# Performance work log

Measured on AMD Instinct MI355X. Metric: run time of the kernel, lower is better.

The kernel has to match this reference:

```python
import jax, jax.numpy as jnp
import numpy as np

D_MODEL, D_INNER, D_STATE, D_CONV, DT_RANK = 2048, 4096, 16, 4, 128
B, T = 2, 1024


def setup_inputs() -> dict:
    key = jax.random.key(0)
    ks = jax.random.split(key, 8)
    dt_init_std = DT_RANK ** -0.5
    # dt bias init per the torch code: inv softplus of dt in [dt_min, dt_max]
    dt = jnp.exp(jax.random.uniform(ks[6], (D_INNER,)) * (np.log(0.1) - np.log(0.001)) + np.log(0.001))
    dt = jnp.clip(dt, 1e-4, None)
    dt_proj_b = dt + jnp.log(-jnp.expm1(-dt))
    A_log = jnp.log(jnp.tile(jnp.arange(1, D_STATE + 1, dtype=jnp.float32)[None, :], (D_INNER, 1)))
    return {
        "x": jax.random.normal(ks[0], (B, T, D_MODEL), jnp.float32),
        "h": jnp.zeros((B, D_INNER, D_STATE), jnp.float32),
        "conv_cache": jnp.zeros((B, D_INNER, D_CONV - 1), jnp.float32),
        "in_proj_w": jax.random.normal(ks[1], (2 * D_INNER, D_MODEL), jnp.float32) * 0.02,
        "conv_w": jax.random.normal(ks[2], (D_INNER, D_CONV), jnp.float32) * (1.0 / np.sqrt(D_CONV)),
        "conv_b": jnp.zeros((D_INNER,), jnp.float32),
        "x_proj_w": jax.random.normal(ks[3], (DT_RANK + 2 * D_STATE, D_INNER), jnp.float32) * 0.02,
        "dt_proj_w": jax.random.uniform(ks[4], (D_INNER, DT_RANK), jnp.float32, -dt_init_std, dt_init_std),
        "dt_proj_b": dt_proj_b,
        "A_log": A_log,
        "D_param": jnp.ones((D_INNER,), jnp.float32),
        "out_proj_w": jax.random.normal(ks[5], (D_MODEL, D_INNER), jnp.float32) * 0.02,
    }


def _forward(x, h, conv_cache, in_proj_w, conv_w, conv_b, x_proj_w,
             dt_proj_w, dt_proj_b, A_log, D_param, out_proj_w):
    Tlen = x.shape[1]
    xz = x @ in_proj_w.T                                  # (B,T,2*d_inner)
    xi, z = jnp.split(xz, 2, axis=-1)
    # causal depthwise conv with cache: concat history then valid conv
    xc = jnp.concatenate([jnp.swapaxes(conv_cache, 1, 2), xi], axis=1)  # (B,T+3,d_inner)
    new_conv_cache = jnp.swapaxes(xc[:, -(D_CONV - 1):, :], 1, 2)       # (B,d_inner,3)
    xconv = sum(xc[:, k:k + Tlen, :] * conv_w[:, k] for k in range(D_CONV)) + conv_b
    xs = jax.nn.silu(xconv)                               # (B,T,d_inner)
    # SSM params per step
    dbc = xs @ x_proj_w.T                                 # (B,T,dt_rank+2n)
    delta, Bm, Cm = jnp.split(dbc, [DT_RANK, DT_RANK + D_STATE], axis=-1)
    delta = jax.nn.softplus(delta @ dt_proj_w.T + dt_proj_b)  # (B,T,d_inner)
    A = -jnp.exp(A_log)                                   # (d_inner,n)
    dA = jnp.exp(jnp.einsum('btd,dn->btdn', delta, A))    # (B,T,d,n)
    dBx = jnp.einsum('btd,btn,btd->btdn', delta, Bm, xs)  # (B,T,d,n)

    def step(hc, inp):
        dA_t, dBx_t, C_t = inp
        hc = dA_t * hc + dBx_t                            # (B,d,n)
        return hc, jnp.einsum('bdn,bn->bd', hc, C_t)

    h_last, ys = jax.lax.scan(
        step, h,
        (jnp.moveaxis(dA, 1, 0), jnp.moveaxis(dBx, 1, 0), jnp.moveaxis(Cm, 1, 0)))
    y = jnp.moveaxis(ys, 0, 1) + D_param * xs             # (B,T,d_inner)
    out = (y * jax.nn.silu(z)) @ out_proj_w.T             # (B,T,d_model)
    return out, h_last, new_conv_cache


def reference(x, h, conv_cache, in_proj_w, conv_w, conv_b, x_proj_w,
              dt_proj_w, dt_proj_b, A_log, D_param, out_proj_w):
    return _forward(x, h, conv_cache, in_proj_w, conv_w, conv_b, x_proj_w,
                    dt_proj_w, dt_proj_b, A_log, D_param, out_proj_w)
```

## Files before the change

### kernel.cpp

```cpp
#include <hip/hip_runtime.h>
#include <hip/hip_bf16.h>
#include <math.h>

#define D_MODEL 2048
#define D_INNER 4096
#define D_STATE 16
#define D_CONV  4
#define DT_RANK 128
#define NB      2
#define TT      1024
#define M_TOT   (NB * TT)
#define NC      16
#define CL      64
#define TC      16

typedef __bf16 bf16x8_t __attribute__((ext_vector_type(8)));
typedef float  f32x4_t  __attribute__((ext_vector_type(4)));

__global__ __launch_bounds__(256) void fused_cast(
    const float* __restrict__ x,  const float* __restrict__ wi,
    const float* __restrict__ wo, const float* __restrict__ wx,
    const float* __restrict__ wdt,
    __bf16* __restrict__ x16,  __bf16* __restrict__ wi16,
    __bf16* __restrict__ wo16, __bf16* __restrict__ wx16,
    __bf16* __restrict__ wdt16, __bf16* __restrict__ dbc16)
{
    const size_t g = (size_t)blockIdx.x * 256 + threadIdx.x;
    const float* src; __bf16* dst; size_t off;
    if      (g < 524288)  { src = x;   dst = x16;   off = g; }
    else if (g < 2621440) { src = wi;  dst = wi16;  off = g - 524288; }
    else if (g < 3670016) { src = wo;  dst = wo16;  off = g - 2621440; }
    else if (g < 3801088) { off = g - 3670016; dst = wx16;
                            src = (g < 3751936) ? wx : nullptr; }
    else if (g < 3866624) { src = wdt; dst = wdt16; off = g - 3801088; }
    else                  { src = nullptr; dst = dbc16; off = g - 3866624; }

    bf16x8_t v;
    if (src) {
        const float4 f0 = ((const float4*)src)[2 * off];
        const float4 f1 = ((const float4*)src)[2 * off + 1];
        v[0] = (__bf16)f0.x; v[1] = (__bf16)f0.y; v[2] = (__bf16)f0.z; v[3] = (__bf16)f0.w;
        v[4] = (__bf16)f1.x; v[5] = (__bf16)f1.y; v[6] = (__bf16)f1.z; v[7] = (__bf16)f1.w;
    } else {
        v = (bf16x8_t)(__bf16)0.f;
    }
    ((bf16x8_t*)dst)[off] = v;
}

__global__ __launch_bounds__(256) void cast_dt16(
    const float* __restrict__ dbc, __bf16* __restrict__ dt16)
{
    int i = blockIdx.x * 256 + threadIdx.x;
    int row = i >> 4, chunk = i & 15;
    const float* s = dbc + (size_t)row * 160 + chunk * 8;
    const float4 f0 = *(const float4*)s;
    const float4 f1 = *(const float4*)(s + 4);
    bf16x8_t v;
    v[0] = (__bf16)f0.x; v[1] = (__bf16)f0.y; v[2] = (__bf16)f0.z; v[3] = (__bf16)f0.w;
    v[4] = (__bf16)f1.x; v[5] = (__bf16)f1.y; v[6] = (__bf16)f1.z; v[7] = (__bf16)f1.w;
    ((bf16x8_t*)(dt16 + (size_t)row * 128))[chunk] = v;
}

template <int EPI, typename OutT>
__global__ __launch_bounds__(256) void gemm_bf16_nt(
    const __bf16* __restrict__ A, int lda,
    const __bf16* __restrict__ W, int ldw,
    OutT* __restrict__ C, int ldc,
    int Kloop, int Nmax, const float* __restrict__ bias)
{
    __shared__ __bf16 As[128 * 32];
    __shared__ __bf16 Bs[128 * 32];

    const int tid  = threadIdx.x;
    const int wave = tid >> 6;
    const int lane = tid & 63;
    const int m0 = blockIdx.y * 128;
    const int n0 = blockIdx.x * 128;
    const int mw = (wave >> 1) * 64;
    const int nw = (wave & 1) * 64;
    const int koff = blockIdx.z * Kloop;

    f32x4_t acc[4][4] = {};

    const int g0 = wave * 2;
    const int rA = g0 * 16 + (lane >> 2);
    const int kk = (lane & 3) * 8;

    const __bf16* gA0 = A + (size_t)(m0 + rA) * lda + kk + koff;
    const __bf16* gA1 = gA0 + (size_t)16 * lda;
    const __bf16* gB0 = W + (size_t)(n0 + rA) * ldw + kk + koff;
    const __bf16* gB1 = gB0 + (size_t)16 * ldw;

    __bf16* lA0 = &As[(size_t)g0 * 512];
    __bf16* lA1 = &As[(size_t)(g0 + 1) * 512];
    __bf16* lB0 = &Bs[(size_t)g0 * 512];
    __bf16* lB1 = &Bs[(size_t)(g0 + 1) * 512];

    const int fr = lane & 15;
    const int fk = (lane >> 4) * 8;

    for (int k0 = 0; k0 < Kloop; k0 += 32) {
        __builtin_amdgcn_global_load_lds(
            (const __attribute__((address_space(1))) void*)(gA0 + k0),
            (__attribute__((address_space(3))) void*)lA0, 16, 0, 0);
        __builtin_amdgcn_global_load_lds(
            (const __attribute__((address_space(1))) void*)(gA1 + k0),
            (__attribute__((address_space(3))) void*)lA1, 16, 0, 0);
        __builtin_amdgcn_global_load_lds(
            (const __attribute__((address_space(1))) void*)(gB0 + k0),
            (__attribute__((address_space(3))) void*)lB0, 16, 0, 0);
        __builtin_amdgcn_global_load_lds(
            (const __attribute__((address_space(1))) void*)(gB1 + k0),
            (__attribute__((address_space(3))) void*)lB1, 16, 0, 0);
        __syncthreads();

        bf16x8_t av[4], bv[4];
#pragma unroll
        for (int mt = 0; mt < 4; mt++)
            av[mt] = *(const bf16x8_t*)&As[(mw + mt * 16 + fr) * 32 + fk];
#pragma unroll
        for (int nt = 0; nt < 4; nt++)
            bv[nt] = *(const bf16x8_t*)&Bs[(nw + nt * 16 + fr) * 32 + fk];

#pragma unroll
        for (int mt = 0; mt < 4; mt++)
#pragma unroll
            for (int nt = 0; nt < 4; nt++)
                acc[mt][nt] = __builtin_amdgcn_mfma_f32_16x16x32_bf16(
                    av[mt], bv[nt], acc[mt][nt], 0, 0, 0);
        __syncthreads();
    }

    const int cn = n0 + nw + (lane & 15);
    const int rb = m0 + mw + (lane >> 4) * 4;
#pragma unroll
    for (int mt = 0; mt < 4; mt++)
#pragma unroll
        for (int nt = 0; nt < 4; nt++) {
            const int n = cn + nt * 16;
            if (n >= Nmax) continue;
#pragma unroll
            for (int r = 0; r < 4; r++) {
                float v = acc[mt][nt][r];
                OutT* p = &C[(size_t)(rb + mt * 16 + r) * ldc + n];
                if (EPI == 1) {
                    v += bias[n];
                    v = (v > 20.f) ? v : log1pf(__expf(v));
                    *p = (OutT)v;
                } else if (EPI == 2) {
                    atomicAdd((float*)p, v);
                } else {
                    *p = (OutT)v;
                }
            }
        }
}

__global__ __launch_bounds__(256) void conv_silu(
    const __bf16* __restrict__ xz16,
    const float* __restrict__ conv_cache,
    const float* __restrict__ conv_w,
    const float* __restrict__ conv_b,
    __bf16* __restrict__ xs16,
    float* __restrict__ cc_out)
{
    const int b  = blockIdx.z;
    const int d  = blockIdx.y * 256 + threadIdx.x;
    const int t0 = blockIdx.x * TC;

    const float4 w  = *(const float4*)&conv_w[d * 4];
    const float bias = conv_b[d];

    float v[TC + 3];
    if (t0 == 0) {
        v[0] = conv_cache[(b * D_INNER + d) * 3 + 0];
        v[1] = conv_cache[(b * D_INNER + d) * 3 + 1];
        v[2] = conv_cache[(b * D_INNER + d) * 3 + 2];
    } else {
        v[0] = (float)xz16[(size_t)(b * TT + t0 - 3) * 8192 + d];
        v[1] = (float)xz16[(size_t)(b * TT + t0 - 2) * 8192 + d];
        v[2] = (float)xz16[(size_t)(b * TT + t0 - 1) * 8192 + d];
    }
#pragma unroll
    for (int k = 0; k < TC; k++)
        v[k + 3] = (float)xz16[(size_t)(b * TT + t0 + k) * 8192 + d];

#pragma unroll
    for (int k = 0; k < TC; k++) {
        float c = v[k] * w.x + v[k + 1] * w.y + v[k + 2] * w.z + v[k + 3] * w.w + bias;
        float s = c / (1.f + __expf(-c));
        xs16[(size_t)(b * TT + t0 + k) * 4096 + d] = (__bf16)s;
    }

    if (t0 + TC == TT) {
        cc_out[(b * D_INNER + d) * 3 + 0] = v[TC];
        cc_out[(b * D_INNER + d) * 3 + 1] = v[TC + 1];
        cc_out[(b * D_INNER + d) * 3 + 2] = v[TC + 2];
    }
}

__global__ __launch_bounds__(256) void scan_phase_a(
    const float* __restrict__ delta_p,
    const float* __restrict__ dbc,
    const __bf16* __restrict__ xs16,
    const float* __restrict__ A_log,
    float* __restrict__ P,
    float* __restrict__ S)
{
    const int idx = blockIdx.x * 256 + threadIdx.x;
    const int sub = idx & 3;
    const int d   = (idx >> 2) & 4095;
    const int c   = (idx >> 14) & (NC - 1);
    const int b   = idx >> 18;

    const float4 Af = *(const float4*)&A_log[d * 16 + sub * 4];
    const float Ad0 = -__expf(Af.x), Ad1 = -__expf(Af.y);
    const float Ad2 = -__expf(Af.z), Ad3 = -__expf(Af.w);

    const int t0 = c * CL;
    const float*  pdelta = delta_p + (size_t)(b * TT + t0) * 4096 + d;
    const __bf16* px     = xs16 + (size_t)(b * TT + t0) * 4096 + d;
    const float*  pB     = dbc + ((size_t)b * TT + t0) * 160 + 128 + sub * 4;

    float h0 = 0.f, h1 = 0.f, h2 = 0.f, h3 = 0.f, sd = 0.f;
    for (int t = 0; t < CL; t++) {
        const float delta = pdelta[(size_t)t * 4096];
        const float xv    = (float)px[(size_t)t * 4096];
        const float4 Bv   = *(const float4*)&pB[(size_t)t * 160];
        const float dx = delta * xv;
        h0 = __expf(delta * Ad0) * h0 + dx * Bv.x;
        h1 = __expf(delta * Ad1) * h1 + dx * Bv.y;
        h2 = __expf(delta * Ad2) * h2 + dx * Bv.z;
        h3 = __expf(delta * Ad3) * h3 + dx * Bv.w;
        sd += delta;
    }
    const size_t o = ((size_t)(b * NC + c) * 4096 + d) * 16 + sub * 4;
    *(float4*)&P[o] = make_float4(__expf(Ad0 * sd), __expf(Ad1 * sd),
                                  __expf(Ad2 * sd), __expf(Ad3 * sd));
    *(float4*)&S[o] = make_float4(h0, h1, h2, h3);
}

__global__ __launch_bounds__(256) void scan_phase_b(
    float* __restrict__ P,
    const float* __restrict__ S,
    const float* __restrict__ h_in,
    float* __restrict__ h_out)
{
    const int idx = blockIdx.x * 256 + threadIdx.x;
    const int n = idx & 15;
    const int d = (idx >> 4) & 4095;
    const int b = idx >> 16;

    float h = h_in[((size_t)b * 4096 + d) * 16 + n];
#pragma unroll
    for (int c = 0; c < NC; c++) {
        const size_t o = ((size_t)(b * NC + c) * 4096 + d) * 16 + n;
        const float p = P[o], s = S[o];
        P[o] = h;
        h = p * h + s;
    }
    h_out[((size_t)b * 4096 + d) * 16 + n] = h;
}

__global__ __launch_bounds__(256) void scan_phase_c(
    const float* __restrict__ delta_p,
    const __bf16* __restrict__ xz16,
    const float* __restrict__ dbc,
    const __bf16* __restrict__ xs16,
    const float* __restrict__ Hs,
    const float* __restrict__ A_log,
    const float* __restrict__ D_param,
    __bf16* __restrict__ ys16)
{
    const int idx = blockIdx.x * 256 + threadIdx.x;
    const int sub = idx & 3;
    const int d   = (idx >> 2) & 4095;
    const int c   = (idx >> 14) & (NC - 1);
    const int b   = idx >> 18;

    const float4 Af = *(const float4*)&A_log[d * 16 + sub * 4];
    const float Ad0 = -__expf(Af.x), Ad1 = -__expf(Af.y);
    const float Ad2 = -__expf(Af.z), Ad3 = -__expf(Af.w);
    const float Dp = D_param[d];

    const size_t o = ((size_t)(b * NC + c) * 4096 + d) * 16 + sub * 4;
    float4 hf = *(const float4*)&Hs[o];
    float h0 = hf.x, h1 = hf.y, h2 = hf.z, h3 = hf.w;

    const int t0 = c * CL;
    const float*  pdelta = delta_p + (size_t)(b * TT + t0) * 4096 + d;
    const __bf16* pz     = xz16 + (size_t)(b * TT + t0) * 8192 + 4096 + d;
    const __bf16* px     = xs16 + (size_t)(b * TT + t0) * 4096 + d;
    const float*  pB     = dbc + ((size_t)b * TT + t0) * 160 + 128 + sub * 4;
    const float*  pC     = pB + 16;
    __bf16* py = ys16 + (size_t)(b * TT + t0) * 4096 + d;

    for (int t = 0; t < CL; t++) {
        const float delta = pdelta[(size_t)t * 4096];
        const float xv    = (float)px[(size_t)t * 4096];
        const float4 Bv   = *(const float4*)&pB[(size_t)t * 160];
        const float4 Cv   = *(const float4*)&pC[(size_t)t * 160];
        const float dx = delta * xv;

        h0 = __expf(delta * Ad0) * h0 + dx * Bv.x;
        h1 = __expf(delta * Ad1) * h1 + dx * Bv.y;
        h2 = __expf(delta * Ad2) * h2 + dx * Bv.z;
        h3 = __expf(delta * Ad3) * h3 + dx * Bv.w;

        float y = h0 * Cv.x + h1 * Cv.y + h2 * Cv.z + h3 * Cv.w;
        y += __shfl_xor(y, 1);
        y += __shfl_xor(y, 2);

        if (sub == 0) {
            const float zv = (float)pz[(size_t)t * 8192];
            y += Dp * xv;
            const float g = zv / (1.f + __expf(-zv));
            py[(size_t)t * 4096] = (__bf16)(y * g);
        }
    }
}

extern "C" void kernel_launch(void* const* d_in, const int* in_sizes, int n_in,
                              void* d_out, int out_size, void* d_ws, size_t ws_size,
                              hipStream_t stream)
{
    const float* x          = (const float*)d_in[0];
    const float* h_in       = (const float*)d_in[1];
    const float* conv_cache = (const float*)d_in[2];
    const float* in_proj_w  = (const float*)d_in[3];
    const float* conv_w     = (const float*)d_in[4];
    const float* conv_b     = (const float*)d_in[5];
    const float* x_proj_w   = (const float*)d_in[6];
    const float* dt_proj_w  = (const float*)d_in[7];
    const float* dt_proj_b  = (const float*)d_in[8];
    const float* A_log      = (const float*)d_in[9];
    const float* D_param    = (const float*)d_in[10];
    const float* out_proj_w = (const float*)d_in[11];

    float* out    = (float*)d_out;
    float* h_out  = (float*)d_out + (size_t)NB * TT * D_MODEL;
    float* cc_out = h_out + (size_t)NB * D_INNER * D_STATE;

    float* Pbuf = out;
    float* Sbuf = out + 2097152;

    char* ws = (char*)d_ws;
    __bf16* xz16  = (__bf16*)(ws);
    __bf16* x16   = (__bf16*)(ws + 33554432);
    __bf16* wi16  = (__bf16*)(ws + 41943040);
    float*  delta = (float*)(ws + 41943040);
    __bf16* wo16  = (__bf16*)(ws + 75497472);
    __bf16* xs16  = (__bf16*)(ws + 92274688);
    float*  dbc   = (float*)(ws + 109051904);
    __bf16* ys16  = (__bf16*)(ws + 110362624);
    __bf16* wx16  = (__bf16*)(ws + 127139840);
    __bf16* dt16  = (__bf16*)(ws + 129236992);
    __bf16* wdt16 = (__bf16*)(ws + 129761280);

    dim3 blk(256);

    fused_cast<<<dim3(15424), blk, 0, stream>>>(
        x, in_proj_w, out_proj_w, x_proj_w, dt_proj_w,
        x16, wi16, wo16, wx16, wdt16, (__bf16*)dbc);

    gemm_bf16_nt<0, __bf16><<<dim3(64, 16, 1), blk, 0, stream>>>(
        x16, 2048, wi16, 2048, xz16, 8192, 2048, 8192, nullptr);

    conv_silu<<<dim3(TT / TC, D_INNER / 256, NB), blk, 0, stream>>>(
        xz16, conv_cache, conv_w, conv_b, xs16, cc_out);

    gemm_bf16_nt<2, float><<<dim3(2, 16, 8), blk, 0, stream>>>(
        xs16, 4096, wx16, 4096, dbc, 160, 512, 160, nullptr);

    cast_dt16<<<dim3(128), blk, 0, stream>>>(dbc, dt16);
    gemm_bf16_nt<1, float><<<dim3(32, 16, 1), blk, 0, stream>>>(
        dt16, 128, wdt16, 128, delta, 4096, 128, 4096, dt_proj_b);

    scan_phase_a<<<dim3(NB * D_INNER * NC * 4 / 256), blk, 0, stream>>>(
        delta, dbc, xs16, A_log, Pbuf, Sbuf);
    scan_phase_b<<<dim3(NB * D_INNER * D_STATE / 256), blk, 0, stream>>>(
        Pbuf, Sbuf, h_in, h_out);
    scan_phase_c<<<dim3(NB * D_INNER * NC * 4 / 256), blk, 0, stream>>>(
        delta, xz16, dbc, xs16, Pbuf, A_log, D_param, ys16);

    hipMemsetAsync(out, 0, (size_t)M_TOT * D_MODEL * 4, stream);
    gemm_bf16_nt<2, float><<<dim3(16, 16, 2), blk, 0, stream>>>(
        ys16, 4096, wo16, 4096, out, 2048, 2048, 2048, nullptr);
}
```

Measured before the change: 512.5 us.

## Fuse dt cast into dt GEMM, merge scan phases, deepen GEMM K-step

Removes the standalone cast_dt16 kernel by converting fp32 dbc to bf16 inside a dedicated dt-projection GEMM. It also folds scan_phase_b into scan_phase_c: each chunk thread recomputes its starting state serially from the P/S chunk summaries, and the last chunk writes h_out. The generic GEMM gains a KSTEP template so in_proj and out_proj load 64-wide K tiles per sync, and out_proj split-K goes from 2 to 4. This saves launches and barriers, at the cost of redundant prefix work in the scan, more atomics in out_proj, and larger LDS tiles.

```diff
diff --git a/kernel.cpp b/kernel.cpp
--- a/kernel.cpp
+++ b/kernel.cpp
@@ -47,29 +47,15 @@
     ((bf16x8_t*)dst)[off] = v;
 }
 
-__global__ __launch_bounds__(256) void cast_dt16(
-    const float* __restrict__ dbc, __bf16* __restrict__ dt16)
-{
-    int i = blockIdx.x * 256 + threadIdx.x;
-    int row = i >> 4, chunk = i & 15;
-    const float* s = dbc + (size_t)row * 160 + chunk * 8;
-    const float4 f0 = *(const float4*)s;
-    const float4 f1 = *(const float4*)(s + 4);
-    bf16x8_t v;
-    v[0] = (__bf16)f0.x; v[1] = (__bf16)f0.y; v[2] = (__bf16)f0.z; v[3] = (__bf16)f0.w;
-    v[4] = (__bf16)f1.x; v[5] = (__bf16)f1.y; v[6] = (__bf16)f1.z; v[7] = (__bf16)f1.w;
-    ((bf16x8_t*)(dt16 + (size_t)row * 128))[chunk] = v;
-}
-
-template <int EPI, typename OutT>
+template <int EPI, int KSTEP, typename OutT>
 __global__ __launch_bounds__(256) void gemm_bf16_nt(
     const __bf16* __restrict__ A, int lda,
     const __bf16* __restrict__ W, int ldw,
     OutT* __restrict__ C, int ldc,
     int Kloop, int Nmax, const float* __restrict__ bias)
 {
-    __shared__ __bf16 As[128 * 32];
-    __shared__ __bf16 Bs[128 * 32];
+    __shared__ __bf16 As[128 * KSTEP];
+    __shared__ __bf16 Bs[128 * KSTEP];
 
     const int tid  = threadIdx.x;
     const int wave = tid >> 6;
@@ -99,35 +85,44 @@
     const int fr = lane & 15;
     const int fk = (lane >> 4) * 8;
 
-    for (int k0 = 0; k0 < Kloop; k0 += 32) {
-        __builtin_amdgcn_global_load_lds(
-            (const __attribute__((address_space(1))) void*)(gA0 + k0),
-            (__attribute__((address_space(3))) void*)lA0, 16, 0, 0);
-        __builtin_amdgcn_global_load_lds(
-            (const __attribute__((address_space(1))) void*)(gA1 + k0),
-            (__attribute__((address_space(3))) void*)lA1, 16, 0, 0);
-        __builtin_amdgcn_global_load_lds(
-            (const __attribute__((address_space(1))) void*)(gB0 + k0),
-            (__attribute__((address_space(3))) void*)lB0, 16, 0, 0);
-        __builtin_amdgcn_global_load_lds(
-            (const __attribute__((address_space(1))) void*)(gB1 + k0),
-            (__attribute__((address_space(3))) void*)lB1, 16, 0, 0);
+    for (int k0 = 0; k0 < Kloop; k0 += KSTEP) {
+#pragma unroll
+        for (int p = 0; p < KSTEP / 32; p++) {
+            const int kp = k0 + p * 32;
+            const int lp = p * 4096;
+            __builtin_amdgcn_global_load_lds(
+                (const __attribute__((address_space(1))) void*)(gA0 + kp),
+                (__attribute__((address_space(3))) void*)(lA0 + lp), 16, 0, 0);
+            __builtin_amdgcn_global_load_lds(
+                (const __attribute__((address_space(1))) void*)(gA1 + kp),
+                (__attribute__((address_space(3))) void*)(lA1 + lp), 16, 0, 0);
+            __builtin_amdgcn_global_load_lds(
+                (const __attribute__((address_space(1))) void*)(gB0 + kp),
+                (__attribute__((address_space(3))) void*)(lB0 + lp), 16, 0, 0);
+            __builtin_amdgcn_global_load_lds(
+                (const __attribute__((address_space(1))) void*)(gB1 + kp),
+                (__attribute__((address_space(3))) void*)(lB1 + lp), 16, 0, 0);
+        }
         __syncthreads();
 
-        bf16x8_t av[4], bv[4];
-#pragma unroll
-        for (int mt = 0; mt < 4; mt++)
-            av[mt] = *(const bf16x8_t*)&As[(mw + mt * 16 + fr) * 32 + fk];
-#pragma unroll
-        for (int nt = 0; nt < 4; nt++)
-            bv[nt] = *(const bf16x8_t*)&Bs[(nw + nt * 16 + fr) * 32 + fk];
-
-#pragma unroll
-        for (int mt = 0; mt < 4; mt++)
+#pragma unroll
+        for (int p = 0; p < KSTEP / 32; p++) {
+            const int lp = p * 4096;
+            bf16x8_t av[4], bv[4];
+#pragma unroll
+            for (int mt = 0; mt < 4; mt++)
+                av[mt] = *(const bf16x8_t*)&As[lp + (mw + mt * 16 + fr) * 32 + fk];
 #pragma unroll
             for (int nt = 0; nt < 4; nt++)
-                acc[mt][nt] = __builtin_amdgcn_mfma_f32_16x16x32_bf16(
-                    av[mt], bv[nt], acc[mt][nt], 0, 0, 0);
+                bv[nt] = *(const bf16x8_t*)&Bs[lp + (nw + nt * 16 + fr) * 32 + fk];
+
+#pragma unroll
+            for (int mt = 0; mt < 4; mt++)
+#pragma unroll
+                for (int nt = 0; nt < 4; nt++)
+                    acc[mt][nt] = __builtin_amdgcn_mfma_f32_16x16x32_bf16(
+                        av[mt], bv[nt], acc[mt][nt], 0, 0, 0);
+        }
         __syncthreads();
     }
 
@@ -156,6 +151,96 @@
         }
 }
 
+__global__ __launch_bounds__(256) void gemm_dt(
+    const float* __restrict__ A,
+    const __bf16* __restrict__ W,
+    float* __restrict__ C,
+    const float* __restrict__ bias)
+{
+    __shared__ __bf16 As[128 * 32];
+    __shared__ __bf16 Bs[128 * 32];
+
+    const int tid  = threadIdx.x;
+    const int wave = tid >> 6;
+    const int lane = tid & 63;
+    const int m0 = blockIdx.y * 128;
+    const int n0 = blockIdx.x * 128;
+    const int mw = (wave >> 1) * 64;
+    const int nw = (wave & 1) * 64;
+
+    f32x4_t acc[4][4] = {};
+
+    const int g0 = wave * 2;
+    const int rA = g0 * 16 + (lane >> 2);
+    const int kk = (lane & 3) * 8;
+
+    const float*  gA0 = A + (size_t)(m0 + rA) * 160 + kk;
+    const float*  gA1 = gA0 + (size_t)16 * 160;
+    const __bf16* gB0 = W + (size_t)(n0 + rA) * 128 + kk;
+    const __bf16* gB1 = gB0 + (size_t)16 * 128;
+
+    __bf16* lA0 = &As[(size_t)g0 * 512];
+    __bf16* lA1 = &As[(size_t)(g0 + 1) * 512];
+    __bf16* lB0 = &Bs[(size_t)g0 * 512];
+    __bf16* lB1 = &Bs[(size_t)(g0 + 1) * 512];
+
+    const int fr = lane & 15;
+    const int fk = (lane >> 4) * 8;
+
+    for (int k0 = 0; k0 < 128; k0 += 32) {
+        const float4 a0 = *(const float4*)(gA0 + k0);
+        const float4 a1 = *(const float4*)(gA0 + k0 + 4);
+        const float4 a2 = *(const float4*)(gA1 + k0);
+        const float4 a3 = *(const float4*)(gA1 + k0 + 4);
+        bf16x8_t va, vb;
+        va[0] = (__bf16)a0.x; va[1] = (__bf16)a0.y; va[2] = (__bf16)a0.z; va[3] = (__bf16)a0.w;
+        va[4] = (__bf16)a1.x; va[5] = (__bf16)a1.y; va[6] = (__bf16)a1.z; va[7] = (__bf16)a1.w;
+        vb[0] = (__bf16)a2.x; vb[1] = (__bf16)a2.y; vb[2] = (__bf16)a2.z; vb[3] = (__bf16)a2.w;
+        vb[4] = (__bf16)a3.x; vb[5] = (__bf16)a3.y; vb[6] = (__bf16)a3.z; vb[7] = (__bf16)a3.w;
+        ((bf16x8_t*)lA0)[lane] = va;
+        ((bf16x8_t*)lA1)[lane] = vb;
+        __builtin_amdgcn_global_load_lds(
+            (const __attribute__((address_space(1))) void*)(gB0 + k0),
+            (__attribute__((address_space(3))) void*)lB0, 16, 0, 0);
+        __builtin_amdgcn_global_load_lds(
+            (const __attribute__((address_space(1))) void*)(gB1 + k0),
+            (__attribute__((address_space(3))) void*)lB1, 16, 0, 0);
+        __syncthreads();
+
+        bf16x8_t av[4], bv[4];
+#pragma unroll
+        for (int mt = 0; mt < 4; mt++)
+            av[mt] = *(const bf16x8_t*)&As[(mw + mt * 16 + fr) * 32 + fk];
+#pragma unroll
+        for (int nt = 0; nt < 4; nt++)
+            bv[nt] = *(const bf16x8_t*)&Bs[(nw + nt * 16 + fr) * 32 + fk];
+
+#pragma unroll
+        for (int mt = 0; mt < 4; mt++)
+#pragma unroll
+            for (int nt = 0; nt < 4; nt++)
+                acc[mt][nt] = __builtin_amdgcn_mfma_f32_16x16x32_bf16(
+                    av[mt], bv[nt], acc[mt][nt], 0, 0, 0);
+        __syncthreads();
+    }
+
+    const int cn = n0 + nw + (lane & 15);
+    const int rb = m0 + mw + (lane >> 4) * 4;
+#pragma unroll
+    for (int mt = 0; mt < 4; mt++)
+#pragma unroll
+        for (int nt = 0; nt < 4; nt++) {
+            const int n = cn + nt * 16;
+            const float bs = bias[n];
+#pragma unroll
+            for (int r = 0; r < 4; r++) {
+                float v = acc[mt][nt][r] + bs;
+                v = (v > 20.f) ? v : log1pf(__expf(v));
+                C[(size_t)(rb + mt * 16 + r) * 4096 + n] = v;
+            }
+        }
+}
+
 __global__ __launch_bounds__(256) void conv_silu(
     const __bf16* __restrict__ xz16,
     const float* __restrict__ conv_cache,
@@ -240,37 +325,18 @@
     *(float4*)&S[o] = make_float4(h0, h1, h2, h3);
 }
 
-__global__ __launch_bounds__(256) void scan_phase_b(
-    float* __restrict__ P,
-    const float* __restrict__ S,
-    const float* __restrict__ h_in,
-    float* __restrict__ h_out)
-{
-    const int idx = blockIdx.x * 256 + threadIdx.x;
-    const int n = idx & 15;
-    const int d = (idx >> 4) & 4095;
-    const int b = idx >> 16;
-
-    float h = h_in[((size_t)b * 4096 + d) * 16 + n];
-#pragma unroll
-    for (int c = 0; c < NC; c++) {
-        const size_t o = ((size_t)(b * NC + c) * 4096 + d) * 16 + n;
-        const float p = P[o], s = S[o];
-        P[o] = h;
-        h = p * h + s;
-    }
-    h_out[((size_t)b * 4096 + d) * 16 + n] = h;
-}
-
 __global__ __launch_bounds__(256) void scan_phase_c(
     const float* __restrict__ delta_p,
     const __bf16* __restrict__ xz16,
     const float* __restrict__ dbc,
     const __bf16* __restrict__ xs16,
-    const float* __restrict__ Hs,
+    const float* __restrict__ P,
+    const float* __restrict__ S,
+    const float* __restrict__ h_in,
     const float* __restrict__ A_log,
     const float* __restrict__ D_param,
-    __bf16* __restrict__ ys16)
+    __bf16* __restrict__ ys16,
+    float* __restrict__ h_out)
 {
     const int idx = blockIdx.x * 256 + threadIdx.x;
     const int sub = idx & 3;
@@ -283,9 +349,17 @@
     const float Ad2 = -__expf(Af.z), Ad3 = -__expf(Af.w);
     const float Dp = D_param[d];
 
-    const size_t o = ((size_t)(b * NC + c) * 4096 + d) * 16 + sub * 4;
-    float4 hf = *(const float4*)&Hs[o];
+    float4 hf = *(const float4*)&h_in[((size_t)b * 4096 + d) * 16 + sub * 4];
     float h0 = hf.x, h1 = hf.y, h2 = hf.z, h3 = hf.w;
+    for (int cc = 0; cc < c; cc++) {
+        const size_t o2 = ((size_t)(b * NC + cc) * 4096 + d) * 16 + sub * 4;
+        const float4 p = *(const float4*)&P[o2];
+        const float4 s = *(const float4*)&S[o2];
+        h0 = p.x * h0 + s.x;
+        h1 = p.y * h1 + s.y;
+        h2 = p.z * h2 + s.z;
+        h3 = p.w * h3 + s.w;
+    }
 
     const int t0 = c * CL;
     const float*  pdelta = delta_p + (size_t)(b * TT + t0) * 4096 + d;
@@ -317,6 +391,11 @@
             const float g = zv / (1.f + __expf(-zv));
             py[(size_t)t * 4096] = (__bf16)(y * g);
         }
+    }
+
+    if (c == NC - 1) {
+        *(float4*)&h_out[((size_t)b * 4096 + d) * 16 + sub * 4] =
+            make_float4(h0, h1, h2, h3);
     }
 }
 
@@ -354,8 +433,7 @@
     float*  dbc   = (float*)(ws + 109051904);
     __bf16* ys16  = (__bf16*)(ws + 110362624);
     __bf16* wx16  = (__bf16*)(ws + 127139840);
-    __bf16* dt16  = (__bf16*)(ws + 129236992);
-    __bf16* wdt16 = (__bf16*)(ws + 129761280);
+    __bf16* wdt16 = (__bf16*)(ws + 129236992);
 
     dim3 blk(256);
 
@@ -363,27 +441,23 @@
         x, in_proj_w, out_proj_w, x_proj_w, dt_proj_w,
         x16, wi16, wo16, wx16, wdt16, (__bf16*)dbc);
 
-    gemm_bf16_nt<0, __bf16><<<dim3(64, 16, 1), blk, 0, stream>>>(
+    gemm_bf16_nt<0, 64, __bf16><<<dim3(64, 16, 1), blk, 0, stream>>>(
         x16, 2048, wi16, 2048, xz16, 8192, 2048, 8192, nullptr);
 
     conv_silu<<<dim3(TT / TC, D_INNER / 256, NB), blk, 0, stream>>>(
         xz16, conv_cache, conv_w, conv_b, xs16, cc_out);
 
-    gemm_bf16_nt<2, float><<<dim3(2, 16, 8), blk, 0, stream>>>(
+    gemm_bf16_nt<2, 32, float><<<dim3(2, 16, 8), blk, 0, stream>>>(
         xs16, 4096, wx16, 4096, dbc, 160, 512, 160, nullptr);
 
-    cast_dt16<<<dim3(128), blk, 0, stream>>>(dbc, dt16);
-    gemm_bf16_nt<1, float><<<dim3(32, 16, 1), blk, 0, stream>>>(
-        dt16, 128, wdt16, 128, delta, 4096, 128, 4096, dt_proj_b);
+    gemm_dt<<<dim3(32, 16), blk, 0, stream>>>(dbc, wdt16, delta, dt_proj_b);
 
     scan_phase_a<<<dim3(NB * D_INNER * NC * 4 / 256), blk, 0, stream>>>(
         delta, dbc, xs16, A_log, Pbuf, Sbuf);
-    scan_phase_b<<<dim3(NB * D_INNER * D_STATE / 256), blk, 0, stream>>>(
-        Pbuf, Sbuf, h_in, h_out);
     scan_phase_c<<<dim3(NB * D_INNER * NC * 4 / 256), blk, 0, stream>>>(
-        delta, xz16, dbc, xs16, Pbuf, A_log, D_param, ys16);
+        delta, xz16, dbc, xs16, Pbuf, Sbuf, h_in, A_log, D_param, ys16, h_out);
 
     hipMemsetAsync(out, 0, (size_t)M_TOT * D_MODEL * 4, stream);
-    gemm_bf16_nt<2, float><<<dim3(16, 16, 2), blk, 0, stream>>>(
-        ys16, 4096, wo16, 4096, out, 2048, 2048, 2048, nullptr);
-}
+    gemm_bf16_nt<2, 64, float><<<dim3(16, 16, 4), blk, 0, stream>>>(
+        ys16, 4096, wo16, 4096, out, 2048, 1024, 2048, nullptr);
+}
```

Result: no change. 504.8 us (-1.5%).
